# Optimization experiments

Measured on AMD Instinct MI355X. Metric: run time of the kernel, lower is better.

## Reference

```python
import jax, jax.numpy as jnp
import numpy as np

B, L1, L2 = 4, 1024, 512
D_PG, D_EX = 2304, 1024
H, HKV, DH = 8, 4, 256
SCALE = 256.0 ** -0.5


def _rope(x, cos, sin):
    # x: [B, L, h, DH]; cos/sin: [B, L, 1, DH//2]
    x = x.astype(jnp.float32)
    x1, x2 = jnp.split(x, 2, axis=-1)
    return jnp.concatenate([x1 * cos - x2 * sin, x2 * cos + x1 * sin], axis=-1)


def setup_inputs() -> dict:
    key = jax.random.key(0)
    ks = jax.random.split(key, 16)
    s = 0.02
    return {
        "pg_embeds": jax.random.normal(ks[0], (B, L1, D_PG), jnp.float32),
        "ex_embeds": jax.random.normal(ks[1], (B, L2, D_EX), jnp.float32),
        "cos": jax.random.normal(ks[2], (B, L1 + L2, 1, DH // 2), jnp.float32),
        "sin": jax.random.normal(ks[3], (B, L1 + L2, 1, DH // 2), jnp.float32),
        "attention_mask": jnp.zeros((B, L1 + L2, L1 + L2), jnp.float32),
        "Wq0": jax.random.normal(ks[4], (H * DH, D_PG), jnp.float32) * s,
        "Wk0": jax.random.normal(ks[5], (HKV * DH, D_PG), jnp.float32) * s,
        "Wv0": jax.random.normal(ks[6], (HKV * DH, D_PG), jnp.float32) * s,
        "Wo0": jax.random.normal(ks[7], (D_PG, H * DH), jnp.float32) * s,
        "Wq1": jax.random.normal(ks[8], (H * DH, D_EX), jnp.float32) * s,
        "Wk1": jax.random.normal(ks[9], (HKV * DH, D_EX), jnp.float32) * s,
        "Wv1": jax.random.normal(ks[10], (HKV * DH, D_EX), jnp.float32) * s,
        "Wo1": jax.random.normal(ks[11], (D_EX, H * DH), jnp.float32) * s,
    }


def reference(pg_embeds, ex_embeds, cos, sin, attention_mask,
              Wq0, Wk0, Wv0, Wo0, Wq1, Wk1, Wv1, Wo1):
    b, l1 = pg_embeds.shape[0], pg_embeds.shape[1]
    l2 = ex_embeds.shape[1]
    # per-stream QKV projections, then concat along sequence
    q = jnp.concatenate([
        (pg_embeds @ Wq0.T).reshape(b, l1, H, DH),
        (ex_embeds @ Wq1.T).reshape(b, l2, H, DH)], axis=1)
    k = jnp.concatenate([
        (pg_embeds @ Wk0.T).reshape(b, l1, HKV, DH),
        (ex_embeds @ Wk1.T).reshape(b, l2, HKV, DH)], axis=1)
    v = jnp.concatenate([
        (pg_embeds @ Wv0.T).reshape(b, l1, HKV, DH),
        (ex_embeds @ Wv1.T).reshape(b, l2, HKV, DH)], axis=1)
    q = _rope(q, cos, sin)  # fp32
    k = _rope(k, cos, sin)
    # GQA: repeat KV heads to match query heads
    rep = H // HKV
    k = jnp.repeat(k, rep, axis=2)
    v = jnp.repeat(jnp.repeat(v, rep, axis=2).astype(jnp.float32), 1, axis=0)
    # scores: [B, H, L, L]
    scores = jnp.einsum('bqhd,bkhd->bhqk', q, k) * SCALE
    scores = scores + attention_mask[:, None, :, :]
    p = jax.nn.softmax(scores, axis=-1)
    att = jnp.einsum('bhqk,bkhd->bqhd', p, v).reshape(b, l1 + l2, H * DH)
    out0 = att[:, :l1] @ Wo0.T
    out1 = att[:, l1:] @ Wo1.T
    return (out0, out1)
```

## Files before the change

### kernel.cpp

```cpp
#include <hip/hip_runtime.h>
#include <stdint.h>
#include <stddef.h>


typedef _Float16 f16;
typedef _Float16 f16x8 __attribute__((ext_vector_type(8)));
typedef _Float16 f16x4 __attribute__((ext_vector_type(4)));
typedef float    f32x4 __attribute__((ext_vector_type(4)));

__device__ __forceinline__ void async_ld16(const void* g, void* l) {
  __builtin_amdgcn_global_load_lds((const __attribute__((address_space(1))) void*)g,
                                   (__attribute__((address_space(3))) void*)l,
                                   16, 0, 0);
}

template <typename Epi>
__device__ __forceinline__ void gemm_core(f16* At, f16* Bt,
                                          const f16* __restrict__ A, int lda,
                                          const f16* __restrict__ Bm, int ldb,
                                          int K, Epi&& epi)
{
  const int t    = threadIdx.x;
  const int w    = t >> 6;
  const int lane = t & 63;
  const int q4   = lane >> 4;
  const int l16  = lane & 15;
  const int wm   = w >> 1;
  const int wn   = w & 1;

  const f32x4 vzero = {0.f, 0.f, 0.f, 0.f};
  f32x4 acc[4][4];
#pragma unroll
  for (int i = 0; i < 4; ++i)
#pragma unroll
    for (int j = 0; j < 4; ++j) acc[i][j] = vzero;

  const int srow = t >> 2;
  const int scol = (t & 3) << 3;
  const f16* aP = A  + (size_t)srow * lda + scol;
  const f16* bP = Bm + (size_t)srow * ldb + scol;
  f16* ldsA0 = At + w * 512;
  f16* ldsA1 = At + 2048 + w * 512;
  f16* ldsB0 = Bt + w * 512;
  f16* ldsB1 = Bt + 2048 + w * 512;
  const size_t a64 = (size_t)64 * lda;
  const size_t b64 = (size_t)64 * ldb;

  for (int k0 = 0; k0 < K; k0 += 32) {
    async_ld16(aP + k0,        ldsA0);
    async_ld16(aP + a64 + k0,  ldsA1);
    async_ld16(bP + k0,        ldsB0);
    async_ld16(bP + b64 + k0,  ldsB1);
    __syncthreads();

    f16x8 af[4], bf[4];
#pragma unroll
    for (int mi = 0; mi < 4; ++mi)
      af[mi] = *(const f16x8*)(At + (wm * 64 + mi * 16 + l16) * 32 + q4 * 8);
#pragma unroll
    for (int ni = 0; ni < 4; ++ni)
      bf[ni] = *(const f16x8*)(Bt + (wn * 64 + ni * 16 + l16) * 32 + q4 * 8);

#pragma unroll
    for (int mi = 0; mi < 4; ++mi)
#pragma unroll
      for (int ni = 0; ni < 4; ++ni)
        acc[mi][ni] = __builtin_amdgcn_mfma_f32_16x16x32_f16(af[mi], bf[ni], acc[mi][ni], 0, 0, 0);
    __syncthreads();
  }

#pragma unroll
  for (int mi = 0; mi < 4; ++mi)
#pragma unroll
    for (int ni = 0; ni < 4; ++ni)
#pragma unroll
      for (int r = 0; r < 4; ++r)
        epi(wm * 64 + mi * 16 + q4 * 4 + r, wn * 64 + ni * 16 + l16, acc[mi][ni][r]);
}

__global__ __launch_bounds__(256) void k_qkv(
    const f16* __restrict__ xpg, const f16* __restrict__ xex,
    const f16* __restrict__ W0,  const f16* __restrict__ W1,
    f16* __restrict__ q, f16* __restrict__ k, f16* __restrict__ v)
{
  __shared__ alignas(16) f16 At[128 * 32];
  __shared__ alignas(16) f16 Bt[128 * 32];
  const int idx = blockIdx.x;
  const bool s0 = idx < 1024;
  int by, bx, K;
  const f16 *A, *B;
  if (s0) { by = idx >> 5; bx = idx & 31; K = 2304;
            A = xpg + (size_t)by * 128 * 2304; B = W0 + (size_t)bx * 128 * 2304; }
  else    { int j = idx - 1024; by = j >> 5; bx = j & 31; K = 1024;
            A = xex + (size_t)by * 128 * 1024; B = W1 + (size_t)bx * 128 * 1024; }
  const int rowbase = by * 128, colbase = bx * 128;
  gemm_core(At, Bt, A, K, B, K, K, [&](int r, int c, float fv) {
    int m = rowbase + r;
    int row = s0 ? ((m >> 10) * 1536 + (m & 1023))
                 : ((m >> 9) * 1536 + 1024 + (m & 511));
    int col = colbase + c;
    f16 h = (f16)fv;
    if      (col < 2048) q[(size_t)row * 2048 + col]        = h;
    else if (col < 3072) k[(size_t)row * 1024 + col - 2048] = h;
    else                 v[(size_t)row * 1024 + col - 3072] = h;
  });
}

__global__ __launch_bounds__(256) void k_rope2(
    f16* __restrict__ q, f16* __restrict__ k,
    const float* __restrict__ cs, const float* __restrict__ sn)
{
  const int tid = blockIdx.x * 256 + threadIdx.x;
  f16* base; int j, bl;
  if (tid < 6291456) {
    j = tid & 127; int h = (tid >> 7) & 7; bl = tid >> 10;
    base = q + ((size_t)bl << 11) + (h << 8);
  } else {
    int t2 = tid - 6291456;
    j = t2 & 127; int h = (t2 >> 7) & 3; bl = t2 >> 9;
    base = k + ((size_t)bl << 10) + (h << 8);
  }
  float x1 = (float)base[j], x2 = (float)base[128 + j];
  float c = cs[(size_t)bl * 128 + j], s = sn[(size_t)bl * 128 + j];
  base[j]       = (f16)(x1 * c - x2 * s);
  base[128 + j] = (f16)(x2 * c + x1 * s);
}

__global__ __launch_bounds__(256) void k_vtrans(const f16* __restrict__ v,
                                                f16* __restrict__ vt)
{
  __shared__ f16 tile[32][33];
  const int b = blockIdx.z;
  const int d0 = blockIdx.x * 32, l0 = blockIdx.y * 32;
  const int t = threadIdx.x;
  const int tr = t >> 5, tc = t & 31;
#pragma unroll
  for (int i = 0; i < 4; ++i) {
    int l = l0 + tr + i * 8;
    tile[tr + i * 8][tc] = v[((size_t)b * 1536 + l) * 1024 + d0 + tc];
  }
  __syncthreads();
#pragma unroll
  for (int i = 0; i < 4; ++i) {
    int d = d0 + tr + i * 8;
    int g = d >> 8, dw = d & 255;
    vt[(((size_t)b * 4 + g) * 256 + dw) * 1536 + l0 + tc] = tile[tc][tr + i * 8];
  }
}

__global__ __launch_bounds__(256) void k_attn(
    const f16* __restrict__ qb, const f16* __restrict__ kb,
    const float* __restrict__ mask, f16* __restrict__ Sdst,
    const f16* __restrict__ Psrc, const f16* __restrict__ vt,
    f16* __restrict__ att0, f16* __restrict__ att1,
    int b_sc, int b_pv, int npv)
{
  __shared__ alignas(16) f16 At[128 * 32];
  __shared__ alignas(16) f16 Bt[128 * 32];
  const int idx = blockIdx.x;
  if (idx < npv) {
    const int h = idx / 24, rem = idx % 24, by = rem >> 1, bx = rem & 1;
    const f16* A = Psrc + (size_t)h * 1536 * 1536 + (size_t)by * 128 * 1536;
    const f16* B = vt + (size_t)(b_pv * 4 + (h >> 1)) * 256 * 1536 + (size_t)bx * 128 * 1536;
    const int rowbase = by * 128, colbase = bx * 128;
    gemm_core(At, Bt, A, 1536, B, 1536, 1536, [&](int r, int c, float fv) {
      int m = rowbase + r;
      if (m < 1024) att0[((size_t)(b_pv * 1024 + m))       * 2048 + h * 256 + colbase + c] = (f16)fv;
      else          att1[((size_t)(b_pv * 512 + m - 1024)) * 2048 + h * 256 + colbase + c] = (f16)fv;
    });
  } else {
    const int j = idx - npv;
    const int h = j / 144, rem = j % 144, by = rem / 12, bx = rem % 12;
    const f16* A = qb + (size_t)b_sc * 1536 * 2048 + h * 256 + (size_t)by * 128 * 2048;
    const f16* B = kb + (size_t)b_sc * 1536 * 1024 + (h >> 1) * 256 + (size_t)bx * 128 * 1024;
    f16* Sz = Sdst + (size_t)h * 1536 * 1536;
    const float* mb = mask + (size_t)b_sc * 1536 * 1536;
    const int rowbase = by * 128, colbase = bx * 128;
    gemm_core(At, Bt, A, 2048, B, 1024, 256, [&](int r, int c, float fv) {
      size_t i = (size_t)(rowbase + r) * 1536 + colbase + c;
      Sz[i] = (f16)(fv * 0.0625f + mb[i]);
    });
  }
}

__global__ __launch_bounds__(256) void k_softmax(f16* __restrict__ S)
{
  const int row = blockIdx.x * 4 + (threadIdx.x >> 6);
  const int lane = threadIdx.x & 63;
  f16* p = S + (size_t)row * 1536 + lane * 8;
  f16x8 v0 = *(const f16x8*)p;
  f16x8 v1 = *(const f16x8*)(p + 512);
  f16x8 v2 = *(const f16x8*)(p + 1024);
  float x[24];
#pragma unroll
  for (int i = 0; i < 8; ++i) {
    x[i] = (float)v0[i]; x[8 + i] = (float)v1[i]; x[16 + i] = (float)v2[i];
  }
  float mx = x[0];
#pragma unroll
  for (int i = 1; i < 24; ++i) mx = fmaxf(mx, x[i]);
#pragma unroll
  for (int o = 32; o > 0; o >>= 1) mx = fmaxf(mx, __shfl_xor(mx, o, 64));
  float s = 0.f;
#pragma unroll
  for (int i = 0; i < 24; ++i) { x[i] = __expf(x[i] - mx); s += x[i]; }
#pragma unroll
  for (int o = 32; o > 0; o >>= 1) s += __shfl_xor(s, o, 64);
  const float inv = 1.f / s;
  f16x8 o0, o1, o2;
#pragma unroll
  for (int i = 0; i < 8; ++i) {
    o0[i] = (f16)(x[i] * inv); o1[i] = (f16)(x[8 + i] * inv); o2[i] = (f16)(x[16 + i] * inv);
  }
  *(f16x8*)p = o0; *(f16x8*)(p + 512) = o1; *(f16x8*)(p + 1024) = o2;
}

__global__ __launch_bounds__(256) void k_oproj(
    const f16* __restrict__ att0, const f16* __restrict__ att1,
    const f16* __restrict__ wo0,  const f16* __restrict__ wo1,
    float* __restrict__ out0, float* __restrict__ out1)
{
  __shared__ alignas(16) f16 At[128 * 32];
  __shared__ alignas(16) f16 Bt[128 * 32];
  const int idx = blockIdx.x;
  int by, bx, ldc;
  const f16 *A, *B;
  float* C;
  if (idx < 576) { by = idx / 18; bx = idx % 18;
                   A = att0 + (size_t)by * 128 * 2048; B = wo0 + (size_t)bx * 128 * 2048;
                   C = out0; ldc = 2304; }
  else           { int j = idx - 576; by = j >> 3; bx = j & 7;
                   A = att1 + (size_t)by * 128 * 2048; B = wo1 + (size_t)bx * 128 * 2048;
                   C = out1; ldc = 1024; }
  const int rowbase = by * 128, colbase = bx * 128;
  gemm_core(At, Bt, A, 2048, B, 2048, 2048, [&](int r, int c, float fv) {
    C[(size_t)(rowbase + r) * ldc + colbase + c] = fv;
  });
}

__global__ __launch_bounds__(256) void k_cast_all(
    const float* __restrict__ s0, const float* __restrict__ s1,
    const float* __restrict__ s2, const float* __restrict__ s3,
    const float* __restrict__ s4, const float* __restrict__ s5,
    const float* __restrict__ s6, const float* __restrict__ s7,
    const float* __restrict__ s8, const float* __restrict__ s9,
    f16* __restrict__ dst)
{
  const size_t gid = ((size_t)blockIdx.x * 256 + threadIdx.x) * 4;
  const float* s; size_t off;
  if      (gid < 9437184ull)  { s = s0; off = gid;               }
  else if (gid < 11534336ull) { s = s1; off = gid - 9437184ull;  }
  else if (gid < 16252928ull) { s = s2; off = gid - 11534336ull; }
  else if (gid < 18612224ull) { s = s3; off = gid - 16252928ull; }
  else if (gid < 20971520ull) { s = s4; off = gid - 18612224ull; }
  else if (gid < 25690112ull) { s = s5; off = gid - 20971520ull; }
  else if (gid < 27787264ull) { s = s6; off = gid - 25690112ull; }
  else if (gid < 28835840ull) { s = s7; off = gid - 27787264ull; }
  else if (gid < 29884416ull) { s = s8; off = gid - 28835840ull; }
  else                        { s = s9; off = gid - 29884416ull; }
  float4 v = *(const float4*)(s + off);
  f16x4 o = {(f16)v.x, (f16)v.y, (f16)v.z, (f16)v.w};
  *(f16x4*)(dst + gid) = o;
}

extern "C" void kernel_launch(void* const* d_in, const int* in_sizes, int n_in,
                              void* d_out, int out_size, void* d_ws, size_t ws_size,
                              hipStream_t stream)
{
  (void)in_sizes; (void)n_in; (void)out_size; (void)ws_size;
  const float* pg  = (const float*)d_in[0];
  const float* ex  = (const float*)d_in[1];
  const float* cs  = (const float*)d_in[2];
  const float* sn  = (const float*)d_in[3];
  const float* msk = (const float*)d_in[4];

  char* ws = (char*)d_ws;
  f16* xpg  = (f16*)(ws + 0);
  f16* xex  = (f16*)(ws + 18874368);
  f16* W0c  = (f16*)(ws + 23068672);
  f16* wo0c = (f16*)(ws + 41943040);
  f16* W1c  = (f16*)(ws + 51380224);
  f16* wo1c = (f16*)(ws + 59768832);
  f16* qb   = (f16*)(ws + 63963136);
  f16* kb   = (f16*)(ws + 89128960);
  f16* vb   = (f16*)(ws + 101711872);
  f16* vt   = (f16*)(ws + 114294784);
  f16* att0 = (f16*)(ws + 126877696);
  f16* att1 = (f16*)(ws + 143654912);
  f16* S0   = (f16*)(ws + 152043520);
  f16* S1   = (f16*)(ws + 189792256);
  float* out0 = (float*)d_out;
  float* out1 = out0 + 9437184;

  k_cast_all<<<31232, 256, 0, stream>>>(
      pg, ex,
      (const float*)d_in[5], (const float*)d_in[6], (const float*)d_in[7],
      (const float*)d_in[8], (const float*)d_in[9], (const float*)d_in[10],
      (const float*)d_in[11], (const float*)d_in[12], (f16*)ws);

  k_qkv<<<1536, 256, 0, stream>>>(xpg, xex, W0c, W1c, qb, kb, vb);

  k_rope2<<<36864, 256, 0, stream>>>(qb, kb, cs, sn);

  k_vtrans<<<dim3(32, 48, 4), 256, 0, stream>>>(vb, vt);

  k_attn<<<1152, 256, 0, stream>>>(qb, kb, msk, S0, S0, vt, att0, att1, 0, 0, 0);
  k_softmax<<<3072, 256, 0, stream>>>(S0);
  k_attn<<<1344, 256, 0, stream>>>(qb, kb, msk, S1, S0, vt, att0, att1, 1, 0, 192);
  k_softmax<<<3072, 256, 0, stream>>>(S1);
  k_attn<<<1344, 256, 0, stream>>>(qb, kb, msk, S0, S1, vt, att0, att1, 2, 1, 192);
  k_softmax<<<3072, 256, 0, stream>>>(S0);
  k_attn<<<1344, 256, 0, stream>>>(qb, kb, msk, S1, S0, vt, att0, att1, 3, 2, 192);
  k_softmax<<<3072, 256, 0, stream>>>(S1);
  k_attn<<<192, 256, 0, stream>>>(qb, kb, msk, S0, S1, vt, att0, att1, 0, 3, 192);

  k_oproj<<<704, 256, 0, stream>>>(att0, att1, wo0c, wo1c, out0, out1);
}
```

Measured before the change: 702.0 us.

## Fuse RoPE into QKV epilogue, cast mask to fp16, overlap final PV with output projection

The separate RoPE pass over q and k is removed. A new weight-cast kernel permutes the rows of Wq/Wk so that each rotary pair (x1_j, x2_j) lands in adjacent columns. The QKV GEMM epilogue then applies the rotation using a lane-xor shuffle, which leaves q and k in a consistently permuted head-dim order that the dot product ignores. The attention mask is cast once to fp16 into the freed W0c workspace, halving the mask bytes reread by every head's score tile. The last batch's PV GEMM is merged with the output projection of batches 0–2 into one launch, with a small trailing launch for batch 3, to cut tail underutilisation at the cost of extra cast launches.

```diff
diff --git a/kernel.cpp b/kernel.cpp
--- a/kernel.cpp
+++ b/kernel.cpp
@@ -81,6 +81,7 @@
 __global__ __launch_bounds__(256) void k_qkv(
     const f16* __restrict__ xpg, const f16* __restrict__ xex,
     const f16* __restrict__ W0,  const f16* __restrict__ W1,
+    const float* __restrict__ cs, const float* __restrict__ sn,
     f16* __restrict__ q, f16* __restrict__ k, f16* __restrict__ v)
 {
   __shared__ alignas(16) f16 At[128 * 32];
@@ -99,31 +100,19 @@
     int row = s0 ? ((m >> 10) * 1536 + (m & 1023))
                  : ((m >> 9) * 1536 + 1024 + (m & 511));
     int col = colbase + c;
-    f16 h = (f16)fv;
-    if      (col < 2048) q[(size_t)row * 2048 + col]        = h;
-    else if (col < 3072) k[(size_t)row * 1024 + col - 2048] = h;
-    else                 v[(size_t)row * 1024 + col - 3072] = h;
+    float p = __shfl_xor(fv, 1, 64);
+    if (col < 3072) {
+      int j = (col & 255) >> 1;
+      float cv = cs[(size_t)row * 128 + j];
+      float sv = sn[(size_t)row * 128 + j];
+      float y = (col & 1) ? (fv * cv + p * sv) : (fv * cv - p * sv);
+      f16 h = (f16)y;
+      if (col < 2048) q[(size_t)row * 2048 + col]        = h;
+      else            k[(size_t)row * 1024 + col - 2048] = h;
+    } else {
+      v[(size_t)row * 1024 + col - 3072] = (f16)fv;
+    }
   });
-}
-
-__global__ __launch_bounds__(256) void k_rope2(
-    f16* __restrict__ q, f16* __restrict__ k,
-    const float* __restrict__ cs, const float* __restrict__ sn)
-{
-  const int tid = blockIdx.x * 256 + threadIdx.x;
-  f16* base; int j, bl;
-  if (tid < 6291456) {
-    j = tid & 127; int h = (tid >> 7) & 7; bl = tid >> 10;
-    base = q + ((size_t)bl << 11) + (h << 8);
-  } else {
-    int t2 = tid - 6291456;
-    j = t2 & 127; int h = (t2 >> 7) & 3; bl = t2 >> 9;
-    base = k + ((size_t)bl << 10) + (h << 8);
-  }
-  float x1 = (float)base[j], x2 = (float)base[128 + j];
-  float c = cs[(size_t)bl * 128 + j], s = sn[(size_t)bl * 128 + j];
-  base[j]       = (f16)(x1 * c - x2 * s);
-  base[128 + j] = (f16)(x2 * c + x1 * s);
 }
 
 __global__ __launch_bounds__(256) void k_vtrans(const f16* __restrict__ v,
@@ -150,7 +139,7 @@
 
 __global__ __launch_bounds__(256) void k_attn(
     const f16* __restrict__ qb, const f16* __restrict__ kb,
-    const float* __restrict__ mask, f16* __restrict__ Sdst,
+    const f16* __restrict__ mask, f16* __restrict__ Sdst,
     const f16* __restrict__ Psrc, const f16* __restrict__ vt,
     f16* __restrict__ att0, f16* __restrict__ att1,
     int b_sc, int b_pv, int npv)
@@ -174,11 +163,11 @@
     const f16* A = qb + (size_t)b_sc * 1536 * 2048 + h * 256 + (size_t)by * 128 * 2048;
     const f16* B = kb + (size_t)b_sc * 1536 * 1024 + (h >> 1) * 256 + (size_t)bx * 128 * 1024;
     f16* Sz = Sdst + (size_t)h * 1536 * 1536;
-    const float* mb = mask + (size_t)b_sc * 1536 * 1536;
+    const f16* mb = mask + (size_t)b_sc * 1536 * 1536;
     const int rowbase = by * 128, colbase = bx * 128;
     gemm_core(At, Bt, A, 2048, B, 1024, 256, [&](int r, int c, float fv) {
       size_t i = (size_t)(rowbase + r) * 1536 + colbase + c;
-      Sz[i] = (f16)(fv * 0.0625f + mb[i]);
+      Sz[i] = (f16)(fv * 0.0625f + (float)mb[i]);
     });
   }
 }
@@ -215,7 +204,47 @@
   *(f16x8*)p = o0; *(f16x8*)(p + 512) = o1; *(f16x8*)(p + 1024) = o2;
 }
 
-__global__ __launch_bounds__(256) void k_oproj(
+__global__ __launch_bounds__(256) void k_tail(
+    const f16* __restrict__ Psrc, const f16* __restrict__ vt,
+    f16* __restrict__ att0, f16* __restrict__ att1,
+    const f16* __restrict__ wo0, const f16* __restrict__ wo1,
+    float* __restrict__ out0, float* __restrict__ out1)
+{
+  __shared__ alignas(16) f16 At[128 * 32];
+  __shared__ alignas(16) f16 Bt[128 * 32];
+  const int idx = blockIdx.x;
+  if (idx < 192) {
+    const int h = idx / 24, rem = idx % 24, by = rem >> 1, bx = rem & 1;
+    const f16* A = Psrc + (size_t)h * 1536 * 1536 + (size_t)by * 128 * 1536;
+    const f16* B = vt + (size_t)(3 * 4 + (h >> 1)) * 256 * 1536 + (size_t)bx * 128 * 1536;
+    const int rowbase = by * 128, colbase = bx * 128;
+    gemm_core(At, Bt, A, 1536, B, 1536, 1536, [&](int r, int c, float fv) {
+      int m = rowbase + r;
+      if (m < 1024) att0[((size_t)(3 * 1024 + m))       * 2048 + h * 256 + colbase + c] = (f16)fv;
+      else          att1[((size_t)(3 * 512 + m - 1024)) * 2048 + h * 256 + colbase + c] = (f16)fv;
+    });
+  } else if (idx < 624) {
+    const int j = idx - 192;
+    const int by = j / 18, bx = j % 18;
+    const f16* A = att0 + (size_t)by * 128 * 2048;
+    const f16* B = wo0 + (size_t)bx * 128 * 2048;
+    const int rowbase = by * 128, colbase = bx * 128;
+    gemm_core(At, Bt, A, 2048, B, 2048, 2048, [&](int r, int c, float fv) {
+      out0[(size_t)(rowbase + r) * 2304 + colbase + c] = fv;
+    });
+  } else {
+    const int j = idx - 624;
+    const int by = j >> 3, bx = j & 7;
+    const f16* A = att1 + (size_t)by * 128 * 2048;
+    const f16* B = wo1 + (size_t)bx * 128 * 2048;
+    const int rowbase = by * 128, colbase = bx * 128;
+    gemm_core(At, Bt, A, 2048, B, 2048, 2048, [&](int r, int c, float fv) {
+      out1[(size_t)(rowbase + r) * 1024 + colbase + c] = fv;
+    });
+  }
+}
+
+__global__ __launch_bounds__(256) void k_oproj3(
     const f16* __restrict__ att0, const f16* __restrict__ att1,
     const f16* __restrict__ wo0,  const f16* __restrict__ wo1,
     float* __restrict__ out0, float* __restrict__ out1)
@@ -226,10 +255,10 @@
   int by, bx, ldc;
   const f16 *A, *B;
   float* C;
-  if (idx < 576) { by = idx / 18; bx = idx % 18;
+  if (idx < 144) { by = 24 + idx / 18; bx = idx % 18;
                    A = att0 + (size_t)by * 128 * 2048; B = wo0 + (size_t)bx * 128 * 2048;
                    C = out0; ldc = 2304; }
-  else           { int j = idx - 576; by = j >> 3; bx = j & 7;
+  else           { int j = idx - 144; by = 12 + (j >> 3); bx = j & 7;
                    A = att1 + (size_t)by * 128 * 2048; B = wo1 + (size_t)bx * 128 * 2048;
                    C = out1; ldc = 1024; }
   const int rowbase = by * 128, colbase = bx * 128;
@@ -242,25 +271,50 @@
     const float* __restrict__ s0, const float* __restrict__ s1,
     const float* __restrict__ s2, const float* __restrict__ s3,
     const float* __restrict__ s4, const float* __restrict__ s5,
-    const float* __restrict__ s6, const float* __restrict__ s7,
-    const float* __restrict__ s8, const float* __restrict__ s9,
-    f16* __restrict__ dst)
+    f16* __restrict__ ws)
 {
   const size_t gid = ((size_t)blockIdx.x * 256 + threadIdx.x) * 4;
-  const float* s; size_t off;
-  if      (gid < 9437184ull)  { s = s0; off = gid;               }
-  else if (gid < 11534336ull) { s = s1; off = gid - 9437184ull;  }
-  else if (gid < 16252928ull) { s = s2; off = gid - 11534336ull; }
-  else if (gid < 18612224ull) { s = s3; off = gid - 16252928ull; }
-  else if (gid < 20971520ull) { s = s4; off = gid - 18612224ull; }
-  else if (gid < 25690112ull) { s = s5; off = gid - 20971520ull; }
-  else if (gid < 27787264ull) { s = s6; off = gid - 25690112ull; }
-  else if (gid < 28835840ull) { s = s7; off = gid - 27787264ull; }
-  else if (gid < 29884416ull) { s = s8; off = gid - 28835840ull; }
-  else                        { s = s9; off = gid - 29884416ull; }
+  const float* s; size_t off, dst;
+  if      (gid < 9437184ull)  { s = s0; off = gid;               dst = 0ull        + off; }
+  else if (gid < 11534336ull) { s = s1; off = gid - 9437184ull;  dst = 9437184ull  + off; }
+  else if (gid < 13893632ull) { s = s2; off = gid - 11534336ull; dst = 18612224ull + off; }
+  else if (gid < 18612224ull) { s = s3; off = gid - 13893632ull; dst = 20971520ull + off; }
+  else if (gid < 19660800ull) { s = s4; off = gid - 18612224ull; dst = 28835840ull + off; }
+  else                        { s = s5; off = gid - 19660800ull; dst = 29884416ull + off; }
   float4 v = *(const float4*)(s + off);
   f16x4 o = {(f16)v.x, (f16)v.y, (f16)v.z, (f16)v.w};
-  *(f16x4*)(dst + gid) = o;
+  *(f16x4*)(ws + dst) = o;
+}
+
+__global__ __launch_bounds__(256) void k_cast_wr(
+    const float* __restrict__ wq0, const float* __restrict__ wk0,
+    const float* __restrict__ wq1, const float* __restrict__ wk1,
+    f16* __restrict__ W0c, f16* __restrict__ W1c)
+{
+  const int idx = blockIdx.x;
+  const float* src; f16* dstm; int K, r, drow;
+  if      (idx < 2048) { src = wq0; dstm = W0c; K = 2304; r = idx;        drow = idx; }
+  else if (idx < 3072) { src = wk0; dstm = W0c; K = 2304; r = idx - 2048; drow = idx; }
+  else if (idx < 5120) { src = wq1; dstm = W1c; K = 1024; r = idx - 3072; drow = idx - 3072; }
+  else                 { src = wk1; dstm = W1c; K = 1024; r = idx - 5120; drow = idx - 3072; }
+  const int w = r & 255;
+  const int srow = (r & ~255) + (w >> 1) + ((w & 1) << 7);
+  const float* sp = src + (size_t)srow * K;
+  f16* dp = dstm + (size_t)drow * K;
+  for (int c = threadIdx.x * 4; c < K; c += 1024) {
+    float4 v = *(const float4*)(sp + c);
+    f16x4 o = {(f16)v.x, (f16)v.y, (f16)v.z, (f16)v.w};
+    *(f16x4*)(dp + c) = o;
+  }
+}
+
+__global__ __launch_bounds__(256) void k_cast_mask(const float* __restrict__ m,
+                                                   f16* __restrict__ mh)
+{
+  const size_t gid = ((size_t)blockIdx.x * 256 + threadIdx.x) * 4;
+  float4 v = *(const float4*)(m + gid);
+  f16x4 o = {(f16)v.x, (f16)v.y, (f16)v.z, (f16)v.w};
+  *(f16x4*)(mh + gid) = o;
 }
 
 extern "C" void kernel_launch(void* const* d_in, const int* in_sizes, int n_in,
@@ -289,30 +343,31 @@
   f16* att1 = (f16*)(ws + 143654912);
   f16* S0   = (f16*)(ws + 152043520);
   f16* S1   = (f16*)(ws + 189792256);
+  f16* mkh  = W0c;
   float* out0 = (float*)d_out;
   float* out1 = out0 + 9437184;
 
-  k_cast_all<<<31232, 256, 0, stream>>>(
-      pg, ex,
-      (const float*)d_in[5], (const float*)d_in[6], (const float*)d_in[7],
-      (const float*)d_in[8], (const float*)d_in[9], (const float*)d_in[10],
+  k_cast_all<<<21248, 256, 0, stream>>>(
+      pg, ex, (const float*)d_in[7], (const float*)d_in[8],
       (const float*)d_in[11], (const float*)d_in[12], (f16*)ws);
-
-  k_qkv<<<1536, 256, 0, stream>>>(xpg, xex, W0c, W1c, qb, kb, vb);
-
-  k_rope2<<<36864, 256, 0, stream>>>(qb, kb, cs, sn);
-
+  k_cast_wr<<<6144, 256, 0, stream>>>(
+      (const float*)d_in[5], (const float*)d_in[6],
+      (const float*)d_in[9], (const float*)d_in[10], W0c, W1c);
+
+  k_qkv<<<1536, 256, 0, stream>>>(xpg, xex, W0c, W1c, cs, sn, qb, kb, vb);
+
+  k_cast_mask<<<9216, 256, 0, stream>>>(msk, mkh);
   k_vtrans<<<dim3(32, 48, 4), 256, 0, stream>>>(vb, vt);
 
-  k_attn<<<1152, 256, 0, stream>>>(qb, kb, msk, S0, S0, vt, att0, att1, 0, 0, 0);
+  k_attn<<<1152, 256, 0, stream>>>(qb, kb, mkh, S0, S0, vt, att0, att1, 0, 0, 0);
   k_softmax<<<3072, 256, 0, stream>>>(S0);
-  k_attn<<<1344, 256, 0, stream>>>(qb, kb, msk, S1, S0, vt, att0, att1, 1, 0, 192);
+  k_attn<<<1344, 256, 0, stream>>>(qb, kb, mkh, S1, S0, vt, att0, att1, 1, 0, 192);
   k_softmax<<<3072, 256, 0, stream>>>(S1);
-  k_attn<<<1344, 256, 0, stream>>>(qb, kb, msk, S0, S1, vt, att0, att1, 2, 1, 192);
+  k_attn<<<1344, 256, 0, stream>>>(qb, kb, mkh, S0, S1, vt, att0, att1, 2, 1, 192);
   k_softmax<<<3072, 256, 0, stream>>>(S0);
-  k_attn<<<1344, 256, 0, stream>>>(qb, kb, msk, S1, S0, vt, att0, att1, 3, 2, 192);
+  k_attn<<<1344, 256, 0, stream>>>(qb, kb, mkh, S1, S0, vt, att0, att1, 3, 2, 192);
   k_softmax<<<3072, 256, 0, stream>>>(S1);
-  k_attn<<<192, 256, 0, stream>>>(qb, kb, msk, S0, S1, vt, att0, att1, 0, 3, 192);
-
-  k_oproj<<<704, 256, 0, stream>>>(att0, att1, wo0c, wo1c, out0, out1);
-}
+
+  k_tail<<<720, 256, 0, stream>>>(S1, vt, att0, att1, wo0c, wo1c, out0, out1);
+  k_oproj3<<<176, 256, 0, stream>>>(att0, att1, wo0c, wo1c, out0, out1);
+}
```

Result: slower. 719.6 us (+2.5%).
